# Optimization experiments

Measured on AMD Instinct MI355X. Metric: run time of the kernel, lower is better.

Reference implementation:

```python
import jax, jax.numpy as jnp
import numpy as np

B, L, D = 32, 8192, 512  # batch, enc_len, 2*hidden_dim

def setup_inputs() -> dict:
    key = jax.random.key(0)
    k1, k2, k3, k4 = jax.random.split(key, 4)
    h_j = jax.random.normal(k1, (B, L, D), dtype=jnp.float32)
    s_i = jax.random.normal(k2, (B, 1, D), dtype=jnp.float32)
    # projector: Linear(4*hidden -> 2*hidden) == (2D -> D); torch weight is [out,in]
    W_proj = jax.random.normal(k3, (D, 2 * D), dtype=jnp.float32) * (1.0 / np.sqrt(2 * D))
    b_proj = jax.random.normal(k4, (D,), dtype=jnp.float32) * 0.01
    return {"h_j": h_j, "s_i": s_i, "W_proj": W_proj, "b_proj": b_proj}

def reference(h_j, s_i, W_proj, b_proj):
    # scores: bmm(h_j, s_i^T) -> [B, L, 1]; softmax over L (dim=1)
    e = jnp.einsum('bld,bqd->blq', h_j, s_i)          # [B, L, 1]
    a = jax.nn.softmax(e, axis=1)                      # [B, L, 1]
    # context: bmm(a^T, h_j) -> [B, 1, D] -> squeeze -> [B, D]
    ctx = jnp.einsum('blq,bld->bqd', a, h_j)[:, 0, :]  # [B, D]
    att = jnp.concatenate([ctx, s_i[:, 0, :]], axis=-1)  # [B, 2D]
    att = jnp.tanh(att)
    att = att @ W_proj.T + b_proj                      # [B, D]
    return (a[:, :, 0], att)
```

## Files before the change

### kernel.cpp

```cpp
#include <hip/hip_runtime.h>
#include <math.h>

#define BB 32
#define LL 8192
#define DD 512
#define CHUNKS 32
#define ROWS_PER_BLOCK (LL / CHUNKS)
#define NCHUNK CHUNKS
#define PSTRIDE (2 + DD)

#define TV_OFF ((size_t)BB * NCHUNK * PSTRIDE)
#define MS_OFF (TV_OFF + (size_t)BB * 1024)

__global__ __launch_bounds__(256) void la_pass1(const float* __restrict__ h,
                                                const float* __restrict__ s,
                                                float* __restrict__ eOut,
                                                float* __restrict__ ws) {
    const int b     = blockIdx.x / CHUNKS;
    const int chunk = blockIdx.x % CHUNKS;
    const int tid   = threadIdx.x;
    const int wave  = tid >> 6;
    const int lane  = tid & 63;

    const float4* s4 = (const float4*)(s + (size_t)b * DD);
    const float4 sv0 = s4[lane];
    const float4 sv1 = s4[lane + 64];

    float m = -INFINITY, ssum = 0.0f;
    float4 c0 = {0.f,0.f,0.f,0.f}, c1 = {0.f,0.f,0.f,0.f};

    const int l0 = chunk * ROWS_PER_BLOCK;
    const float4* hbase = (const float4*)(h + (size_t)b * LL * DD);

    for (int r = wave; r < ROWS_PER_BLOCK; r += 4) {
        const int l = l0 + r;
        const float4* hrow = hbase + (size_t)l * (DD / 4);
        float4 h0 = hrow[lane];
        float4 h1 = hrow[lane + 64];
        float dot = h0.x*sv0.x + h0.y*sv0.y + h0.z*sv0.z + h0.w*sv0.w
                  + h1.x*sv1.x + h1.y*sv1.y + h1.z*sv1.z + h1.w*sv1.w;
        #pragma unroll
        for (int off = 32; off > 0; off >>= 1) dot += __shfl_xor(dot, off, 64);
        if (lane == 0) eOut[(size_t)b * LL + l] = dot;
        float mn   = fmaxf(m, dot);
        float corr = __expf(m - mn);
        float p    = __expf(dot - mn);
        ssum = ssum * corr + p;
        c0.x = c0.x*corr + p*h0.x;  c0.y = c0.y*corr + p*h0.y;
        c0.z = c0.z*corr + p*h0.z;  c0.w = c0.w*corr + p*h0.w;
        c1.x = c1.x*corr + p*h1.x;  c1.y = c1.y*corr + p*h1.y;
        c1.z = c1.z*corr + p*h1.z;  c1.w = c1.w*corr + p*h1.w;
        m = mn;
    }

    __shared__ float lm[4], ls[4];
    __shared__ float lctx[4][DD];
    lctx[wave][4*lane + 0] = c0.x;  lctx[wave][4*lane + 1] = c0.y;
    lctx[wave][4*lane + 2] = c0.z;  lctx[wave][4*lane + 3] = c0.w;
    lctx[wave][256 + 4*lane + 0] = c1.x;  lctx[wave][256 + 4*lane + 1] = c1.y;
    lctx[wave][256 + 4*lane + 2] = c1.z;  lctx[wave][256 + 4*lane + 3] = c1.w;
    if (lane == 0) { lm[wave] = m; ls[wave] = ssum; }
    __syncthreads();

    const float mb = fmaxf(fmaxf(lm[0], lm[1]), fmaxf(lm[2], lm[3]));
    const float w0 = __expf(lm[0] - mb), w1 = __expf(lm[1] - mb);
    const float w2 = __expf(lm[2] - mb), w3 = __expf(lm[3] - mb);
    const float sb = ls[0]*w0 + ls[1]*w1 + ls[2]*w2 + ls[3]*w3;

    float* p = ws + ((size_t)b * NCHUNK + chunk) * PSTRIDE;
    if (tid == 0) { p[0] = mb; p[1] = sb; }
    p[2 + tid]       = lctx[0][tid]*w0       + lctx[1][tid]*w1       + lctx[2][tid]*w2       + lctx[3][tid]*w3;
    p[2 + 256 + tid] = lctx[0][256+tid]*w0   + lctx[1][256+tid]*w1   + lctx[2][256+tid]*w2   + lctx[3][256+tid]*w3;
}

__global__ __launch_bounds__(256) void la_pass2(const float* __restrict__ s,
                                                float* __restrict__ ws) {
    const int b = blockIdx.x;
    const int t = threadIdx.x;
    __shared__ float cm[NCHUNK], cs[NCHUNK], cw[NCHUNK];
    const float* pb = ws + (size_t)b * NCHUNK * PSTRIDE;
    if (t < NCHUNK) {
        cm[t] = pb[(size_t)t * PSTRIDE];
        cs[t] = pb[(size_t)t * PSTRIDE + 1];
    }
    __syncthreads();
    float mb = -INFINITY;
    for (int c = 0; c < NCHUNK; ++c) mb = fmaxf(mb, cm[c]);
    float sb = 0.0f;
    for (int c = 0; c < NCHUNK; ++c) sb += cs[c] * __expf(cm[c] - mb);
    if (t < NCHUNK) cw[t] = __expf(cm[t] - mb);
    __syncthreads();
    const float rcp = 1.0f / sb;

    float acc0 = 0.0f, acc1 = 0.0f;
    for (int c = 0; c < NCHUNK; ++c) {
        const float* pc = pb + (size_t)c * PSTRIDE + 2;
        acc0 += cw[c] * pc[t];
        acc1 += cw[c] * pc[t + 256];
    }
    float* tv = ws + TV_OFF + (size_t)b * 1024;
    tv[t]             = tanhf(acc0 * rcp);
    tv[t + 256]       = tanhf(acc1 * rcp);
    tv[512 + t]       = tanhf(s[(size_t)b * DD + t]);
    tv[512 + t + 256] = tanhf(s[(size_t)b * DD + t + 256]);
    if (t == 0) { ws[MS_OFF + 2*b] = mb; ws[MS_OFF + 2*b + 1] = rcp; }
}

__global__ __launch_bounds__(256) void la_pass3(float* __restrict__ out,
                                                const float* __restrict__ ws) {
    const int i4 = blockIdx.x * 256 + threadIdx.x;
    const int b  = i4 >> 11;
    const float mb  = ws[MS_OFF + 2*b];
    const float rcp = ws[MS_OFF + 2*b + 1];
    float4* o4 = (float4*)out;
    float4 e = o4[i4];
    e.x = __expf(e.x - mb) * rcp;
    e.y = __expf(e.y - mb) * rcp;
    e.z = __expf(e.z - mb) * rcp;
    e.w = __expf(e.w - mb) * rcp;
    o4[i4] = e;
}

__global__ __launch_bounds__(256) void la_pass4(const float* __restrict__ W,
                                                const float* __restrict__ bias,
                                                const float* __restrict__ ws,
                                                float* __restrict__ attOut) {
    const int wv   = blockIdx.x * 4 + (threadIdx.x >> 6);
    const int lane = threadIdx.x & 63;
    const int b = wv >> 9;
    const int o = wv & 511;
    const float4* w4 = (const float4*)(W + (size_t)o * 1024);
    const float4* t4 = (const float4*)(ws + TV_OFF + (size_t)b * 1024);
    float acc = 0.0f;
    #pragma unroll
    for (int j = 0; j < 4; ++j) {
        float4 wl = w4[lane + 64*j];
        float4 tl = t4[lane + 64*j];
        acc += wl.x*tl.x + wl.y*tl.y + wl.z*tl.z + wl.w*tl.w;
    }
    #pragma unroll
    for (int off = 32; off > 0; off >>= 1) acc += __shfl_xor(acc, off, 64);
    if (lane == 0) attOut[(size_t)b * DD + o] = acc + bias[o];
}

extern "C" void kernel_launch(void* const* d_in, const int* in_sizes, int n_in,
                              void* d_out, int out_size, void* d_ws, size_t ws_size,
                              hipStream_t stream) {
    const float* h_j    = (const float*)d_in[0];
    const float* s_i    = (const float*)d_in[1];
    const float* W_proj = (const float*)d_in[2];
    const float* b_proj = (const float*)d_in[3];
    float* out = (float*)d_out;
    float* ws  = (float*)d_ws;

    float* eOut   = out;
    float* attOut = out + (size_t)BB * LL;

    la_pass1<<<BB * CHUNKS, 256, 0, stream>>>(h_j, s_i, eOut, ws);
    la_pass2<<<BB, 256, 0, stream>>>(s_i, ws);
    la_pass3<<<(BB * LL / 4) / 256, 256, 0, stream>>>(out, ws);
    la_pass4<<<(BB * DD / 4), 256, 0, stream>>>(W_proj, b_proj, ws, attOut);
}
```

Baseline: 688.2 us.

## Process two rows per wave with dual softmax accumulators and double chunk count

Each wave now loads and reduces two rows per iteration, keeping two independent online-softmax states that are merged at the end. This puts more memory loads in flight and breaks the serial dependency chain through the running max. The online update is branchy, so only one exp is needed per row. The number of L-chunks is doubled to 64 to launch more blocks. Scores are staged in shared memory and written out coalesced at the end of the block, and the larger workspace must still fit in the provided buffer.

```diff
diff --git a/kernel.cpp b/kernel.cpp
--- a/kernel.cpp
+++ b/kernel.cpp
@@ -4,13 +4,19 @@
 #define BB 32
 #define LL 8192
 #define DD 512
-#define CHUNKS 32
+#define CHUNKS 64
 #define ROWS_PER_BLOCK (LL / CHUNKS)
 #define NCHUNK CHUNKS
 #define PSTRIDE (2 + DD)
 
 #define TV_OFF ((size_t)BB * NCHUNK * PSTRIDE)
 #define MS_OFF (TV_OFF + (size_t)BB * 1024)
+
+__device__ __forceinline__ float dot8(const float4& x0, const float4& x1,
+                                      const float4& y0, const float4& y1) {
+    return x0.x*y0.x + x0.y*y0.y + x0.z*y0.z + x0.w*y0.w
+         + x1.x*y1.x + x1.y*y1.y + x1.z*y1.z + x1.w*y1.w;
+}
 
 __global__ __launch_bounds__(256) void la_pass1(const float* __restrict__ h,
                                                 const float* __restrict__ s,
@@ -26,51 +32,91 @@
     const float4 sv0 = s4[lane];
     const float4 sv1 = s4[lane + 64];
 
-    float m = -INFINITY, ssum = 0.0f;
-    float4 c0 = {0.f,0.f,0.f,0.f}, c1 = {0.f,0.f,0.f,0.f};
+    float mA = -INFINITY, sA = 0.0f;
+    float4 a0 = {0.f,0.f,0.f,0.f}, a1 = {0.f,0.f,0.f,0.f};
+    float mB = -INFINITY, sB = 0.0f;
+    float4 b0 = {0.f,0.f,0.f,0.f}, b1 = {0.f,0.f,0.f,0.f};
+
+    __shared__ float esc[ROWS_PER_BLOCK];
+    __shared__ float lm[4], lsum[4];
+    __shared__ float lctx[4][DD];
 
     const int l0 = chunk * ROWS_PER_BLOCK;
-    const float4* hbase = (const float4*)(h + (size_t)b * LL * DD);
-
-    for (int r = wave; r < ROWS_PER_BLOCK; r += 4) {
-        const int l = l0 + r;
-        const float4* hrow = hbase + (size_t)l * (DD / 4);
-        float4 h0 = hrow[lane];
-        float4 h1 = hrow[lane + 64];
-        float dot = h0.x*sv0.x + h0.y*sv0.y + h0.z*sv0.z + h0.w*sv0.w
-                  + h1.x*sv1.x + h1.y*sv1.y + h1.z*sv1.z + h1.w*sv1.w;
+    const float4* hbase = (const float4*)(h + ((size_t)b * LL + l0) * DD);
+
+    for (int i = 0; i < ROWS_PER_BLOCK / 8; ++i) {
+        const int r0 = i * 8 + wave * 2;
+        const float4* row0 = hbase + (size_t)r0 * (DD / 4);
+        const float4* row1 = row0 + (DD / 4);
+        float4 h00 = row0[lane];
+        float4 h01 = row0[lane + 64];
+        float4 h10 = row1[lane];
+        float4 h11 = row1[lane + 64];
+        float d0 = dot8(h00, h01, sv0, sv1);
+        float d1 = dot8(h10, h11, sv0, sv1);
         #pragma unroll
-        for (int off = 32; off > 0; off >>= 1) dot += __shfl_xor(dot, off, 64);
-        if (lane == 0) eOut[(size_t)b * LL + l] = dot;
-        float mn   = fmaxf(m, dot);
-        float corr = __expf(m - mn);
-        float p    = __expf(dot - mn);
-        ssum = ssum * corr + p;
-        c0.x = c0.x*corr + p*h0.x;  c0.y = c0.y*corr + p*h0.y;
-        c0.z = c0.z*corr + p*h0.z;  c0.w = c0.w*corr + p*h0.w;
-        c1.x = c1.x*corr + p*h1.x;  c1.y = c1.y*corr + p*h1.y;
-        c1.z = c1.z*corr + p*h1.z;  c1.w = c1.w*corr + p*h1.w;
-        m = mn;
-    }
-
-    __shared__ float lm[4], ls[4];
-    __shared__ float lctx[4][DD];
-    lctx[wave][4*lane + 0] = c0.x;  lctx[wave][4*lane + 1] = c0.y;
-    lctx[wave][4*lane + 2] = c0.z;  lctx[wave][4*lane + 3] = c0.w;
-    lctx[wave][256 + 4*lane + 0] = c1.x;  lctx[wave][256 + 4*lane + 1] = c1.y;
-    lctx[wave][256 + 4*lane + 2] = c1.z;  lctx[wave][256 + 4*lane + 3] = c1.w;
-    if (lane == 0) { lm[wave] = m; ls[wave] = ssum; }
+        for (int off = 32; off > 0; off >>= 1) {
+            d0 += __shfl_xor(d0, off, 64);
+            d1 += __shfl_xor(d1, off, 64);
+        }
+        if (lane == 0) { esc[r0] = d0; esc[r0 + 1] = d1; }
+
+        if (d0 <= mA) {
+            float p = __expf(d0 - mA);
+            sA += p;
+            a0.x += p*h00.x; a0.y += p*h00.y; a0.z += p*h00.z; a0.w += p*h00.w;
+            a1.x += p*h01.x; a1.y += p*h01.y; a1.z += p*h01.z; a1.w += p*h01.w;
+        } else {
+            float c = __expf(mA - d0);
+            sA = sA*c + 1.0f;
+            a0.x = a0.x*c + h00.x; a0.y = a0.y*c + h00.y;
+            a0.z = a0.z*c + h00.z; a0.w = a0.w*c + h00.w;
+            a1.x = a1.x*c + h01.x; a1.y = a1.y*c + h01.y;
+            a1.z = a1.z*c + h01.z; a1.w = a1.w*c + h01.w;
+            mA = d0;
+        }
+        if (d1 <= mB) {
+            float p = __expf(d1 - mB);
+            sB += p;
+            b0.x += p*h10.x; b0.y += p*h10.y; b0.z += p*h10.z; b0.w += p*h10.w;
+            b1.x += p*h11.x; b1.y += p*h11.y; b1.z += p*h11.z; b1.w += p*h11.w;
+        } else {
+            float c = __expf(mB - d1);
+            sB = sB*c + 1.0f;
+            b0.x = b0.x*c + h10.x; b0.y = b0.y*c + h10.y;
+            b0.z = b0.z*c + h10.z; b0.w = b0.w*c + h10.w;
+            b1.x = b1.x*c + h11.x; b1.y = b1.y*c + h11.y;
+            b1.z = b1.z*c + h11.z; b1.w = b1.w*c + h11.w;
+            mB = d1;
+        }
+    }
+
+    const float mw = fmaxf(mA, mB);
+    const float wa = __expf(mA - mw), wb = __expf(mB - mw);
+    const float sw = sA*wa + sB*wb;
+    a0.x = a0.x*wa + b0.x*wb; a0.y = a0.y*wa + b0.y*wb;
+    a0.z = a0.z*wa + b0.z*wb; a0.w = a0.w*wa + b0.w*wb;
+    a1.x = a1.x*wa + b1.x*wb; a1.y = a1.y*wa + b1.y*wb;
+    a1.z = a1.z*wa + b1.z*wb; a1.w = a1.w*wa + b1.w*wb;
+
+    lctx[wave][4*lane + 0] = a0.x;  lctx[wave][4*lane + 1] = a0.y;
+    lctx[wave][4*lane + 2] = a0.z;  lctx[wave][4*lane + 3] = a0.w;
+    lctx[wave][256 + 4*lane + 0] = a1.x;  lctx[wave][256 + 4*lane + 1] = a1.y;
+    lctx[wave][256 + 4*lane + 2] = a1.z;  lctx[wave][256 + 4*lane + 3] = a1.w;
+    if (lane == 0) { lm[wave] = mw; lsum[wave] = sw; }
     __syncthreads();
 
-    const float mb = fmaxf(fmaxf(lm[0], lm[1]), fmaxf(lm[2], lm[3]));
-    const float w0 = __expf(lm[0] - mb), w1 = __expf(lm[1] - mb);
-    const float w2 = __expf(lm[2] - mb), w3 = __expf(lm[3] - mb);
-    const float sb = ls[0]*w0 + ls[1]*w1 + ls[2]*w2 + ls[3]*w3;
+    const float mb_ = fmaxf(fmaxf(lm[0], lm[1]), fmaxf(lm[2], lm[3]));
+    const float w0 = __expf(lm[0] - mb_), w1 = __expf(lm[1] - mb_);
+    const float w2 = __expf(lm[2] - mb_), w3 = __expf(lm[3] - mb_);
+    const float sb_ = lsum[0]*w0 + lsum[1]*w1 + lsum[2]*w2 + lsum[3]*w3;
 
     float* p = ws + ((size_t)b * NCHUNK + chunk) * PSTRIDE;
-    if (tid == 0) { p[0] = mb; p[1] = sb; }
-    p[2 + tid]       = lctx[0][tid]*w0       + lctx[1][tid]*w1       + lctx[2][tid]*w2       + lctx[3][tid]*w3;
-    p[2 + 256 + tid] = lctx[0][256+tid]*w0   + lctx[1][256+tid]*w1   + lctx[2][256+tid]*w2   + lctx[3][256+tid]*w3;
+    if (tid == 0) { p[0] = mb_; p[1] = sb_; }
+    p[2 + tid]       = lctx[0][tid]*w0     + lctx[1][tid]*w1     + lctx[2][tid]*w2     + lctx[3][tid]*w3;
+    p[2 + 256 + tid] = lctx[0][256+tid]*w0 + lctx[1][256+tid]*w1 + lctx[2][256+tid]*w2 + lctx[3][256+tid]*w3;
+
+    if (tid < ROWS_PER_BLOCK) eOut[(size_t)b * LL + l0 + tid] = esc[tid];
 }
 
 __global__ __launch_bounds__(256) void la_pass2(const float* __restrict__ s,
```

Result: no change. 697.0 us (+1.3%).
